# Kernel tuning notes

Measured on AMD Instinct MI355X. Metric: run time of the kernel, lower is better.

Reference implementation:

```python
import jax, jax.numpy as jnp
import numpy as np

M, K, N = 32, 4096, 12288


def setup_inputs() -> dict:
    key = jax.random.key(0)
    k1, k2, k3, k4 = jax.random.split(key, 4)
    x = jax.random.normal(k1, (M, K), dtype=jnp.float32)
    # uint8-valued packed weight (stored as int32 for harness compatibility, values in [0,256))
    weight_u8 = jax.random.randint(k2, (K, N), 0, 256, dtype=jnp.int32)
    # per-output-channel fp16 scale and zero-point
    scale = (jax.random.uniform(k3, (N,), dtype=jnp.float32) * 0.01 + 1e-3).astype(jnp.float16)
    zero = (jax.random.uniform(k4, (N,), dtype=jnp.float32) * 255.0).astype(jnp.float16)
    return {"x": x, "weight_u8": weight_u8, "scale": scale, "zero": zero}


def reference(x, weight_u8, scale, zero):
    # QuantMatmulCustom: dequantize uint8 weight with per-channel fp16 scale/zero, then matmul.
    # w_deq[k, n] = (w_u8[k, n] - zero[n]) * scale[n]
    w_deq = (weight_u8.astype(jnp.float32) - zero.astype(jnp.float32)[None, :]) * scale.astype(jnp.float32)[None, :]
    # [M, K] @ [K, N] -> [M, N]
    return jnp.einsum('mk,kn->mn', x, w_deq)
```

## Files before the change

### kernel.cpp

```cpp
#include <hip/hip_runtime.h>

#define M_DIM 32
#define K_DIM 4096
#define N_DIM 12288
#define SPLITK 16
#define KPER  (K_DIM / SPLITK)
#define NT    (KPER / 32)
#define BLK   512
#define NPB   128

using bf16x8 = __attribute__((ext_vector_type(8))) short;
using f32x4  = __attribute__((ext_vector_type(4))) float;

__device__ __forceinline__ void load_b(const int* __restrict__ wp, int t, int (&wv)[8]) {
    #pragma unroll
    for (int j = 0; j < 8; ++j)
        wv[j] = wp[(size_t)(t * 32 + j) * N_DIM];
}

__device__ __forceinline__ bf16x8 pack_b(const int (&wv)[8]) {
    bf16x8 b;
    #pragma unroll
    for (int j = 0; j < 8; ++j) {
        float f = (float)wv[j];
        b[j] = (short)(__float_as_uint(f) >> 16);
    }
    return b;
}

template <bool WS>
__global__ __launch_bounds__(BLK, 4) void qmm_main(const float* __restrict__ x,
                                                   const int* __restrict__ w,
                                                   float* __restrict__ dst) {
    __shared__ short lds_a[NT * 2 * 64 * 8];

    const int tid  = threadIdx.x;
    const int lane = tid & 63;
    const int g    = lane >> 4;
    const int c    = lane & 15;
    const int wid  = tid >> 6;
    const int k0   = blockIdx.y * KPER;
    const int n0   = blockIdx.x * NPB + wid * 16;

    for (int s = tid; s < NT * 2 * 64; s += BLK) {
        const int l  = s & 63;
        const int h  = (s >> 6) & 1;
        const int kt = s >> 7;
        const int m  = 16 * h + (l & 15);
        const float* xp = x + (size_t)m * K_DIM + k0 + kt * 32 + 8 * (l >> 4);
        bf16x8 v;
        #pragma unroll
        for (int j = 0; j < 8; ++j) {
            unsigned u = __float_as_uint(xp[j]);
            u += 0x7FFFu + ((u >> 16) & 1u);
            v[j] = (short)(u >> 16);
        }
        *(bf16x8*)&lds_a[s * 8] = v;
    }

    const int*   wp = w + (size_t)(k0 + 8 * g) * N_DIM + n0 + c;
    const short* la = lds_a + lane * 8;

    int wv[3][8];
    load_b(wp, 0, wv[0]);
    load_b(wp, 1, wv[1]);
    load_b(wp, 2, wv[2]);
    __syncthreads();

    f32x4 acc0 = {0.f, 0.f, 0.f, 0.f};
    f32x4 acc1 = {0.f, 0.f, 0.f, 0.f};

    #pragma unroll
    for (int t = 0; t < NT; ++t) {
        bf16x8 bf = pack_b(wv[t % 3]);
        if (t + 3 < NT) load_b(wp, t + 3, wv[t % 3]);
        bf16x8 a0 = *(const bf16x8*)&la[(size_t)(t * 2 + 0) * 512];
        bf16x8 a1 = *(const bf16x8*)&la[(size_t)(t * 2 + 1) * 512];
        acc0 = __builtin_amdgcn_mfma_f32_16x16x32_bf16(a0, bf, acc0, 0, 0, 0);
        acc1 = __builtin_amdgcn_mfma_f32_16x16x32_bf16(a1, bf, acc1, 0, 0, 0);
    }

    if (WS) {
        float* pp = dst + ((size_t)blockIdx.y * M_DIM) * N_DIM + n0 + c;
        #pragma unroll
        for (int i = 0; i < 4; ++i) {
            const int r = 4 * (lane >> 4) + i;
            pp[(size_t)r * N_DIM]        = acc0[i];
            pp[(size_t)(16 + r) * N_DIM] = acc1[i];
        }
    } else {
        #pragma unroll
        for (int i = 0; i < 4; ++i) {
            const int r = 4 * (lane >> 4) + i;
            atomicAdd(&dst[(size_t)r * N_DIM + n0 + c], acc0[i]);
            atomicAdd(&dst[(size_t)(16 + r) * N_DIM + n0 + c], acc1[i]);
        }
    }
}

__global__ __launch_bounds__(256) void qmm_finalize(const float* __restrict__ part,
                                                    const float* __restrict__ x,
                                                    const float* __restrict__ scale,
                                                    const float* __restrict__ zero,
                                                    float* __restrict__ out) {
    const int m = blockIdx.y;
    __shared__ float red[256];
    float s = 0.f;
    for (int k = threadIdx.x; k < K_DIM; k += 256)
        s += x[(size_t)m * K_DIM + k];
    red[threadIdx.x] = s;
    __syncthreads();
    #pragma unroll
    for (int off = 128; off > 0; off >>= 1) {
        if (threadIdx.x < off) red[threadIdx.x] += red[threadIdx.x + off];
        __syncthreads();
    }
    const float rowsum = red[0];

    const int n = blockIdx.x * 256 + threadIdx.x;
    float acc = 0.f;
    #pragma unroll
    for (int sp = 0; sp < SPLITK; ++sp)
        acc += part[((size_t)sp * M_DIM + m) * N_DIM + n];
    out[(size_t)m * N_DIM + n] = scale[n] * (acc - zero[n] * rowsum);
}

__global__ __launch_bounds__(256) void qmm_zero(float* __restrict__ out) {
    int i = blockIdx.x * 256 + threadIdx.x;
    ((float4*)out)[i] = make_float4(0.f, 0.f, 0.f, 0.f);
}
__global__ __launch_bounds__(256) void qmm_scale(const float* __restrict__ x,
                                                 const float* __restrict__ scale,
                                                 const float* __restrict__ zero,
                                                 float* __restrict__ out) {
    const int m = blockIdx.y;
    __shared__ float red[256];
    float s = 0.f;
    for (int k = threadIdx.x; k < K_DIM; k += 256)
        s += x[(size_t)m * K_DIM + k];
    red[threadIdx.x] = s;
    __syncthreads();
    #pragma unroll
    for (int off = 128; off > 0; off >>= 1) {
        if (threadIdx.x < off) red[threadIdx.x] += red[threadIdx.x + off];
        __syncthreads();
    }
    const float rowsum = red[0];
    const int n = blockIdx.x * 256 + threadIdx.x;
    const float v = out[(size_t)m * N_DIM + n];
    out[(size_t)m * N_DIM + n] = scale[n] * (v - zero[n] * rowsum);
}

extern "C" void kernel_launch(void* const* d_in, const int* in_sizes, int n_in,
                              void* d_out, int out_size, void* d_ws, size_t ws_size,
                              hipStream_t stream) {
    const float* x     = (const float*)d_in[0];
    const int*   w     = (const int*)d_in[1];
    const float* scale = (const float*)d_in[2];
    const float* zero  = (const float*)d_in[3];
    float* out = (float*)d_out;

    const size_t need = (size_t)SPLITK * M_DIM * N_DIM * sizeof(float);
    if (ws_size >= need) {
        float* part = (float*)d_ws;
        qmm_main<true><<<dim3(N_DIM / NPB, SPLITK), dim3(BLK), 0, stream>>>(x, w, part);
        qmm_finalize<<<dim3(N_DIM / 256, M_DIM),    dim3(256), 0, stream>>>(part, x, scale, zero, out);
    } else {
        qmm_zero <<<dim3((M_DIM * N_DIM / 4) / 256),  dim3(256), 0, stream>>>(out);
        qmm_main<false><<<dim3(N_DIM / NPB, SPLITK),  dim3(BLK), 0, stream>>>(x, w, out);
        qmm_scale<<<dim3(N_DIM / 256, M_DIM),         dim3(256), 0, stream>>>(x, scale, zero, out);
    }
}
```

Baseline: 48.59 us.

## Stage weight tiles through LDS with async global_load_lds and vectorize finalize

The main kernel now loads uint8-in-int32 weight tiles with global_load_lds into a swizzled, double-buffered LDS buffer instead of strided per-lane global loads, so weight reads become 16-byte coalesced. Each warp then reads its columns from LDS, with a block-wide barrier every k-step. The per-row sum of x moves into a separate small kernel computed once per row, and finalize reads partials, scale and zero as float4. Risks include the extra barrier per iteration, more LDS per block (which may limit occupancy), and an added kernel launch.

```diff
diff --git a/kernel.cpp b/kernel.cpp
--- a/kernel.cpp
+++ b/kernel.cpp
@@ -12,11 +12,8 @@
 using bf16x8 = __attribute__((ext_vector_type(8))) short;
 using f32x4  = __attribute__((ext_vector_type(4))) float;
 
-__device__ __forceinline__ void load_b(const int* __restrict__ wp, int t, int (&wv)[8]) {
-    #pragma unroll
-    for (int j = 0; j < 8; ++j)
-        wv[j] = wp[(size_t)(t * 32 + j) * N_DIM];
-}
+typedef __attribute__((address_space(1))) const void GASV;
+typedef __attribute__((address_space(3))) void LASV;
 
 __device__ __forceinline__ bf16x8 pack_b(const int (&wv)[8]) {
     bf16x8 b;
@@ -33,6 +30,7 @@
                                                    const int* __restrict__ w,
                                                    float* __restrict__ dst) {
     __shared__ short lds_a[NT * 2 * 64 * 8];
+    __shared__ int   lds_b[2][32 * 128];
 
     const int tid  = threadIdx.x;
     const int lane = tid & 63;
@@ -40,7 +38,26 @@
     const int c    = lane & 15;
     const int wid  = tid >> 6;
     const int k0   = blockIdx.y * KPER;
-    const int n0   = blockIdx.x * NPB + wid * 16;
+    const int n0   = blockIdx.x * NPB;
+    const int n0w  = n0 + wid * 16;
+
+    const int* gsrc[2];
+    #pragma unroll
+    for (int q = 0; q < 2; ++q) {
+        const int i     = wid * 2 + q;
+        const int r     = 2 * i + (lane >> 5);
+        const int nslot = 4 * (lane & 31);
+        const int col   = nslot ^ (((r >> 3) & 1) << 4);
+        gsrc[q] = w + (size_t)(k0 + r) * N_DIM + n0 + col;
+    }
+
+    #pragma unroll
+    for (int q = 0; q < 2; ++q) {
+        __builtin_amdgcn_global_load_lds((GASV*)gsrc[q],
+                                         (LASV*)&lds_b[0][(wid * 2 + q) * 256], 16, 0, 0);
+        __builtin_amdgcn_global_load_lds((GASV*)(gsrc[q] + (size_t)32 * N_DIM),
+                                         (LASV*)&lds_b[1][(wid * 2 + q) * 256], 16, 0, 0);
+    }
 
     for (int s = tid; s < NT * 2 * 64; s += BLK) {
         const int l  = s & 63;
@@ -57,31 +74,38 @@
         }
         *(bf16x8*)&lds_a[s * 8] = v;
     }
-
-    const int*   wp = w + (size_t)(k0 + 8 * g) * N_DIM + n0 + c;
-    const short* la = lds_a + lane * 8;
-
-    int wv[3][8];
-    load_b(wp, 0, wv[0]);
-    load_b(wp, 1, wv[1]);
-    load_b(wp, 2, wv[2]);
     __syncthreads();
 
     f32x4 acc0 = {0.f, 0.f, 0.f, 0.f};
     f32x4 acc1 = {0.f, 0.f, 0.f, 0.f};
 
+    const short* la     = lds_a + lane * 8;
+    const int    colrd  = (wid * 16 + c) ^ ((g & 1) << 4);
+
     #pragma unroll
     for (int t = 0; t < NT; ++t) {
-        bf16x8 bf = pack_b(wv[t % 3]);
-        if (t + 3 < NT) load_b(wp, t + 3, wv[t % 3]);
+        const int* bb = &lds_b[t & 1][g * 8 * 128 + colrd];
+        int wv[8];
+        #pragma unroll
+        for (int j = 0; j < 8; ++j) wv[j] = bb[j * 128];
+        bf16x8 bf = pack_b(wv);
         bf16x8 a0 = *(const bf16x8*)&la[(size_t)(t * 2 + 0) * 512];
         bf16x8 a1 = *(const bf16x8*)&la[(size_t)(t * 2 + 1) * 512];
         acc0 = __builtin_amdgcn_mfma_f32_16x16x32_bf16(a0, bf, acc0, 0, 0, 0);
         acc1 = __builtin_amdgcn_mfma_f32_16x16x32_bf16(a1, bf, acc1, 0, 0, 0);
+
+        __syncthreads();
+        if (t + 2 < NT) {
+            #pragma unroll
+            for (int q = 0; q < 2; ++q)
+                __builtin_amdgcn_global_load_lds(
+                    (GASV*)(gsrc[q] + (size_t)32 * (t + 2) * N_DIM),
+                    (LASV*)&lds_b[t & 1][(wid * 2 + q) * 256], 16, 0, 0);
+        }
     }
 
     if (WS) {
-        float* pp = dst + ((size_t)blockIdx.y * M_DIM) * N_DIM + n0 + c;
+        float* pp = dst + ((size_t)blockIdx.y * M_DIM) * N_DIM + n0w + c;
         #pragma unroll
         for (int i = 0; i < 4; ++i) {
             const int r = 4 * (lane >> 4) + i;
@@ -92,37 +116,55 @@
         #pragma unroll
         for (int i = 0; i < 4; ++i) {
             const int r = 4 * (lane >> 4) + i;
-            atomicAdd(&dst[(size_t)r * N_DIM + n0 + c], acc0[i]);
-            atomicAdd(&dst[(size_t)(16 + r) * N_DIM + n0 + c], acc1[i]);
-        }
-    }
+            atomicAdd(&dst[(size_t)r * N_DIM + n0w + c], acc0[i]);
+            atomicAdd(&dst[(size_t)(16 + r) * N_DIM + n0w + c], acc1[i]);
+        }
+    }
+}
+
+__global__ __launch_bounds__(256) void qmm_rowsum(const float* __restrict__ x,
+                                                  float* __restrict__ rowsum) {
+    const int m = blockIdx.x;
+    __shared__ float red[256];
+    const float4* xp = (const float4*)(x + (size_t)m * K_DIM);
+    float s = 0.f;
+    #pragma unroll
+    for (int i = 0; i < K_DIM / 4 / 256; ++i) {
+        float4 v = xp[threadIdx.x + 256 * i];
+        s += v.x + v.y + v.z + v.w;
+    }
+    red[threadIdx.x] = s;
+    __syncthreads();
+    #pragma unroll
+    for (int off = 128; off > 0; off >>= 1) {
+        if (threadIdx.x < off) red[threadIdx.x] += red[threadIdx.x + off];
+        __syncthreads();
+    }
+    if (threadIdx.x == 0) rowsum[m] = red[0];
 }
 
 __global__ __launch_bounds__(256) void qmm_finalize(const float* __restrict__ part,
-                                                    const float* __restrict__ x,
+                                                    const float* __restrict__ rowsum,
                                                     const float* __restrict__ scale,
                                                     const float* __restrict__ zero,
                                                     float* __restrict__ out) {
-    const int m = blockIdx.y;
-    __shared__ float red[256];
-    float s = 0.f;
-    for (int k = threadIdx.x; k < K_DIM; k += 256)
-        s += x[(size_t)m * K_DIM + k];
-    red[threadIdx.x] = s;
-    __syncthreads();
-    #pragma unroll
-    for (int off = 128; off > 0; off >>= 1) {
-        if (threadIdx.x < off) red[threadIdx.x] += red[threadIdx.x + off];
-        __syncthreads();
-    }
-    const float rowsum = red[0];
-
-    const int n = blockIdx.x * 256 + threadIdx.x;
-    float acc = 0.f;
-    #pragma unroll
-    for (int sp = 0; sp < SPLITK; ++sp)
-        acc += part[((size_t)sp * M_DIM + m) * N_DIM + n];
-    out[(size_t)m * N_DIM + n] = scale[n] * (acc - zero[n] * rowsum);
+    const int m  = blockIdx.y;
+    const int n4 = blockIdx.x * 256 + threadIdx.x;
+    const float rs = rowsum[m];
+    float4 acc = make_float4(0.f, 0.f, 0.f, 0.f);
+    #pragma unroll
+    for (int sp = 0; sp < SPLITK; ++sp) {
+        float4 p = ((const float4*)(part + ((size_t)sp * M_DIM + m) * N_DIM))[n4];
+        acc.x += p.x; acc.y += p.y; acc.z += p.z; acc.w += p.w;
+    }
+    const float4 sc = ((const float4*)scale)[n4];
+    const float4 zp = ((const float4*)zero)[n4];
+    float4 o;
+    o.x = sc.x * (acc.x - zp.x * rs);
+    o.y = sc.y * (acc.y - zp.y * rs);
+    o.z = sc.z * (acc.z - zp.z * rs);
+    o.w = sc.w * (acc.w - zp.w * rs);
+    ((float4*)(out + (size_t)m * N_DIM))[n4] = o;
 }
 
 __global__ __launch_bounds__(256) void qmm_zero(float* __restrict__ out) {
@@ -160,11 +202,14 @@
     const float* zero  = (const float*)d_in[3];
     float* out = (float*)d_out;
 
-    const size_t need = (size_t)SPLITK * M_DIM * N_DIM * sizeof(float);
+    const size_t part_sz = (size_t)SPLITK * M_DIM * N_DIM * sizeof(float);
+    const size_t need    = part_sz + M_DIM * sizeof(float);
     if (ws_size >= need) {
-        float* part = (float*)d_ws;
+        float* part   = (float*)d_ws;
+        float* rowsum = (float*)((char*)d_ws + part_sz);
         qmm_main<true><<<dim3(N_DIM / NPB, SPLITK), dim3(BLK), 0, stream>>>(x, w, part);
-        qmm_finalize<<<dim3(N_DIM / 256, M_DIM),    dim3(256), 0, stream>>>(part, x, scale, zero, out);
+        qmm_rowsum    <<<dim3(M_DIM),               dim3(256), 0, stream>>>(x, rowsum);
+        qmm_finalize  <<<dim3(N_DIM / 4 / 256, M_DIM), dim3(256), 0, stream>>>(part, rowsum, scale, zero, out);
     } else {
         qmm_zero <<<dim3((M_DIM * N_DIM / 4) / 256),  dim3(256), 0, stream>>>(out);
         qmm_main<false><<<dim3(N_DIM / NPB, SPLITK),  dim3(BLK), 0, stream>>>(x, w, out);
```

After: 45.99 us. 1.06x faster.
